# Kernel optimization log

Measured on AMD Instinct MI355X. Metric: run time of the kernel, lower is better.

## Reference

```python
import jax, jax.numpy as jnp
import numpy as np

B = 131072
H_GAS = 8
H_EXT = 16
# gas order and net counts, total 99 tiny MLPs
GAS_SIZES = [23, 29, 13, 9, 3, 9, 13]  # h2o, h2o_sq, o3, co2, n2o, ch4, u
N_NETS = 29

# index maps taken verbatim from the 29 tau_gases assignment lines
H2O_ROWS = np.arange(23)
H2O_IDX = np.array([0,1,2,3,4,5,6,3,4,9,10,11,12,13,14,15,16,17,18,19,20,21,22])
O3_ROWS = np.array([0,1,2,17,18,19,20,21,22,25,26,27,28])
CO2_ROWS = np.array([0,1,2,5,6,9,10,13,14])
N2O_ROWS = np.array([0,1,2])
CH4_ROWS = np.array([0,1,2,3,4,7,8,11,12])
U_ROWS = np.array([0,1,2,15,16,17,18,19,20,21,22,27,28])


def setup_inputs() -> dict:
    key = jax.random.key(0)
    ks = jax.random.split(key, 23)
    f = jnp.float32
    inp = {
        'temp': jax.random.normal(ks[0], (B, 1), f),
        'pressure': jax.random.normal(ks[1], (B, 1), f),
        'comp_h2o': jax.random.uniform(ks[2], (B, 1), f),
        'comp_h2o_sq': jax.random.uniform(ks[3], (B, 1), f),
        'comp_o3': jax.random.uniform(ks[4], (B, 1), f),
        'comp_co2': jax.random.uniform(ks[5], (B, 1), f),
        'comp_n2o': jax.random.uniform(ks[6], (B, 1), f),
        'comp_ch4': jax.random.uniform(ks[7], (B, 1), f),
        'comp_u': jax.random.uniform(ks[8], (B, 1), f),
        'lwp': jax.random.uniform(ks[9], (B, 1), f, minval=0.05, maxval=1.0),
        'iwp': jax.random.uniform(ks[10], (B, 1), f, minval=0.05, maxval=1.0),
        'mu': jax.random.uniform(ks[11], (B, 1), f, minval=0.1, maxval=1.0),
        'mu_bar': jax.random.uniform(ks[12], (B, 1), f, minval=0.1, maxval=1.0),
        'gas_W1': jax.random.normal(ks[13], (99, 2, H_GAS), f) * 0.5,
        'gas_b1': jax.random.normal(ks[14], (99, H_GAS), f) * 0.1,
        'gas_W2': jax.random.normal(ks[15], (99, H_GAS, 1), f) * 0.5,
        'gas_b2': jax.random.uniform(ks[16], (99, 1), f, minval=0.05, maxval=0.5),
        'lw_w': jax.random.uniform(ks[17], (N_NETS, 1), f, minval=0.05, maxval=1.0),
        'iw_w': jax.random.uniform(ks[18], (N_NETS, 1), f, minval=0.05, maxval=1.0),
        'ext_W1': jax.random.normal(ks[19], (N_NETS, 4, H_EXT), f) * 0.5,
        'ext_b1': jax.random.normal(ks[20], (N_NETS, H_EXT), f) * 0.1,
        'ext_W2': jax.random.normal(ks[21], (N_NETS, H_EXT, 3), f) * 0.5,
        'ext_b2': jax.random.normal(ks[22], (N_NETS, 3), f) * 0.1,
    }
    return inp


def reference(temp, pressure, comp_h2o, comp_h2o_sq, comp_o3, comp_co2, comp_n2o,
              comp_ch4, comp_u, lwp, iwp, mu, mu_bar,
              gas_W1, gas_b1, gas_W2, gas_b2, lw_w, iw_w,
              ext_W1, ext_b1, ext_W2, ext_b2):
    b = temp.shape[0]
    X = jnp.concatenate([temp, pressure], axis=-1)              # [B,2]
    # all 99 per-gas tiny MLPs in one batched pass
    h = jax.nn.elu(jnp.einsum('bi,nih->nbh', X, gas_W1) + gas_b1[:, None, :])
    ke = jax.nn.relu(jnp.einsum('nbh,nho->nbo', h, gas_W2) + gas_b2[:, None, :])[..., 0]  # [99,B]
    comps = [comp_h2o, comp_h2o_sq, comp_o3, comp_co2, comp_n2o, comp_ch4, comp_u]
    comp_all = jnp.concatenate(
        [jnp.broadcast_to(c[:, 0][None, :], (n, b)) for c, n in zip(comps, GAS_SIZES)], axis=0)
    tau_all = ke * comp_all                                      # [99,B]
    h2o    = tau_all[0:23]
    h2o_sq = tau_all[23:52]
    o3     = tau_all[52:65]
    co2    = tau_all[65:74]
    n2o    = tau_all[74:77]
    ch4    = tau_all[77:86]
    u      = tau_all[86:99]
    # scatter-combine into the 29 spectral channels
    tau_g = h2o_sq                                               # every row has h2o_sq[k]
    tau_g = tau_g.at[H2O_ROWS].add(h2o[H2O_IDX])
    tau_g = tau_g.at[O3_ROWS].add(o3)
    tau_g = tau_g.at[CO2_ROWS].add(co2)
    tau_g = tau_g.at[N2O_ROWS].add(n2o)
    tau_g = tau_g.at[CH4_ROWS].add(ch4)
    tau_g = tau_g.at[U_ROWS].add(u)
    tau_lw = lw_w * lwp[:, 0][None, :]                           # [29,B]
    tau_iw = iw_w * iwp[:, 0][None, :]
    tau_total = tau_g + tau_lw + tau_iw
    in1 = tau_lw / tau_total
    in2 = tau_iw / tau_total
    mu_v, mub_v = mu[:, 0], mu_bar[:, 0]
    in3_dir = tau_total / mu_v[None, :]
    in3_dif = tau_total / mub_v[None, :]

    def ext(i1, i2, i3, m):
        Xe = jnp.stack([i1, i2, i3, jnp.broadcast_to(m[None, :], i1.shape)], axis=-1)  # [29,B,4]
        he = jax.nn.elu(jnp.einsum('nbi,nih->nbh', Xe, ext_W1) + ext_b1[:, None, :])
        return jax.nn.relu(jnp.einsum('nbh,nho->nbo', he, ext_W2) + ext_b2[:, None, :])

    e_direct = jax.nn.softmax(ext(in1, in2, in3_dir, mu_v), axis=-1)   # [29,B,3]
    e_diffuse = jax.nn.softmax(ext(in1, in2, in3_dif, mub_v), axis=-1)
    t_direct = jnp.exp(-in3_dir)
    t_diffuse = jnp.exp(-in3_dif)
    return (t_direct, t_diffuse, e_direct, e_diffuse)
```

## Files before the change

kernel.cpp:

```cpp
#include <hip/hip_runtime.h>
#include <math.h>

#define TPB 256

static __device__ const int ROW_START[30] = {
    0, 7, 14, 21, 24, 27, 30, 33, 36, 39, 42, 45, 48, 51, 54, 57, 60,
    63, 67, 71, 75, 79, 83, 87, 88, 89, 91, 93, 96, 99};

static __device__ const unsigned char NET_ID[99] = {
    23, 0, 52, 65, 74, 77, 86,
    24, 1, 53, 66, 75, 78, 87,
    25, 2, 54, 67, 76, 79, 88,
    26, 3, 80,
    27, 4, 81,
    28, 5, 68,
    29, 6, 69,
    30, 3, 82,
    31, 4, 83,
    32, 9, 70,
    33, 10, 71,
    34, 11, 84,
    35, 12, 85,
    36, 13, 72,
    37, 14, 73,
    38, 15, 89,
    39, 16, 90,
    40, 17, 55, 91,
    41, 18, 56, 92,
    42, 19, 57, 93,
    43, 20, 58, 94,
    44, 21, 59, 95,
    45, 22, 60, 96,
    46,
    47,
    48, 61,
    49, 62,
    50, 63, 97,
    51, 64, 98};

static __device__ const unsigned char COMP_ID[99] = {
    1, 0, 2, 3, 4, 5, 6,
    1, 0, 2, 3, 4, 5, 6,
    1, 0, 2, 3, 4, 5, 6,
    1, 0, 5,
    1, 0, 5,
    1, 0, 3,
    1, 0, 3,
    1, 0, 5,
    1, 0, 5,
    1, 0, 3,
    1, 0, 3,
    1, 0, 5,
    1, 0, 5,
    1, 0, 3,
    1, 0, 3,
    1, 0, 6,
    1, 0, 6,
    1, 0, 2, 6,
    1, 0, 2, 6,
    1, 0, 2, 6,
    1, 0, 2, 6,
    1, 0, 2, 6,
    1, 0, 2, 6,
    1,
    1,
    1, 2,
    1, 2,
    1, 2, 6,
    1, 2, 6};

__device__ __forceinline__ float fast_rcp(float x) {
    return __builtin_amdgcn_rcpf(x);
}

__global__ __launch_bounds__(TPB) void atm_kernel(
    const float* __restrict__ temp,
    const float* __restrict__ pressure,
    const float* __restrict__ c_h2o,
    const float* __restrict__ c_h2o_sq,
    const float* __restrict__ c_o3,
    const float* __restrict__ c_co2,
    const float* __restrict__ c_n2o,
    const float* __restrict__ c_ch4,
    const float* __restrict__ c_u,
    const float* __restrict__ lwp,
    const float* __restrict__ iwp,
    const float* __restrict__ mu,
    const float* __restrict__ mu_bar,
    const float* __restrict__ gW1,
    const float* __restrict__ gb1,
    const float* __restrict__ gW2,
    const float* __restrict__ gb2,
    const float* __restrict__ lw_w,
    const float* __restrict__ iw_w,
    const float* __restrict__ eW1,
    const float* __restrict__ eb1,
    const float* __restrict__ eW2,
    const float* __restrict__ eb2,
    float* __restrict__ out,
    int Bn)
{
    const int r = blockIdx.x;
    const int b = blockIdx.y * TPB + threadIdx.x;
    if (b >= Bn) return;

    const float t = temp[b];
    const float p = pressure[b];
    float comp[7];
    comp[0] = c_h2o[b];
    comp[1] = c_h2o_sq[b];
    comp[2] = c_o3[b];
    comp[3] = c_co2[b];
    comp[4] = c_n2o[b];
    comp[5] = c_ch4[b];
    comp[6] = c_u[b];
    const float lwp_b = lwp[b], iwp_b = iwp[b];
    const float mu_b = mu[b], mub_b = mu_bar[b];

    float tau_g = 0.f;
    const int i0 = ROW_START[r], i1 = ROW_START[r + 1];
    for (int i = i0; i < i1; ++i) {
        const int n = NET_ID[i];
        const float* w1 = gW1 + n * 16;
        const float* b1 = gb1 + n * 8;
        const float* w2 = gW2 + n * 8;
        float acc = gb2[n];
        #pragma unroll
        for (int j = 0; j < 8; ++j) {
            float h = fmaf(t, w1[j], fmaf(p, w1[8 + j], b1[j]));
            h = h > 0.f ? h : (__expf(h) - 1.f);
            acc = fmaf(h, w2[j], acc);
        }
        acc = fmaxf(acc, 0.f);
        tau_g = fmaf(acc, comp[COMP_ID[i]], tau_g);
    }

    const float tlw = lw_w[r] * lwp_b;
    const float tiw = iw_w[r] * iwp_b;
    const float tau_tot = tau_g + tlw + tiw;
    const float inv_tt = fast_rcp(tau_tot);
    const float in1 = tlw * inv_tt;
    const float in2 = tiw * inv_tt;
    const float in3_dir = tau_tot * fast_rcp(mu_b);
    const float in3_dif = tau_tot * fast_rcp(mub_b);

    const size_t idx = (size_t)r * (size_t)Bn + (size_t)b;
    out[idx] = __expf(-in3_dir);
    out[(size_t)29 * Bn + idx] = __expf(-in3_dif);

    const float* w1 = eW1 + r * 64;
    const float* b1 = eb1 + r * 16;
    const float* w2 = eW2 + r * 48;
    const float* b2 = eb2 + r * 3;

    float res[6];
    #pragma unroll
    for (int pass = 0; pass < 2; ++pass) {
        const float i3 = (pass == 0) ? in3_dir : in3_dif;
        const float m  = (pass == 0) ? mu_b : mub_b;
        float o0 = b2[0], o1 = b2[1], o2 = b2[2];
        #pragma unroll
        for (int j = 0; j < 16; ++j) {
            float h = fmaf(in1, w1[j], b1[j]);
            h = fmaf(in2, w1[16 + j], h);
            h = fmaf(i3,  w1[32 + j], h);
            h = fmaf(m,   w1[48 + j], h);
            h = h > 0.f ? h : (__expf(h) - 1.f);
            o0 = fmaf(h, w2[3 * j + 0], o0);
            o1 = fmaf(h, w2[3 * j + 1], o1);
            o2 = fmaf(h, w2[3 * j + 2], o2);
        }
        o0 = fmaxf(o0, 0.f);
        o1 = fmaxf(o1, 0.f);
        o2 = fmaxf(o2, 0.f);
        const float mx = fmaxf(o0, fmaxf(o1, o2));
        const float e0 = __expf(o0 - mx);
        const float e1 = __expf(o1 - mx);
        const float e2 = __expf(o2 - mx);
        const float rs = fast_rcp(e0 + e1 + e2);
        res[pass * 3 + 0] = e0 * rs;
        res[pass * 3 + 1] = e1 * rs;
        res[pass * 3 + 2] = e2 * rs;
    }

    float* pd = out + (size_t)58 * Bn + idx * 3;
    pd[0] = res[0]; pd[1] = res[1]; pd[2] = res[2];
    float* pf = out + (size_t)145 * Bn + idx * 3;
    pf[0] = res[3]; pf[1] = res[4]; pf[2] = res[5];
}

extern "C" void kernel_launch(void* const* d_in, const int* in_sizes, int n_in,
                              void* d_out, int out_size, void* d_ws, size_t ws_size,
                              hipStream_t stream) {
    const int Bn = in_sizes[0];
    dim3 grid(29, (Bn + TPB - 1) / TPB);
    atm_kernel<<<grid, TPB, 0, stream>>>(
        (const float*)d_in[0],  (const float*)d_in[1],  (const float*)d_in[2],
        (const float*)d_in[3],  (const float*)d_in[4],  (const float*)d_in[5],
        (const float*)d_in[6],  (const float*)d_in[7],  (const float*)d_in[8],
        (const float*)d_in[9],  (const float*)d_in[10], (const float*)d_in[11],
        (const float*)d_in[12], (const float*)d_in[13], (const float*)d_in[14],
        (const float*)d_in[15], (const float*)d_in[16], (const float*)d_in[17],
        (const float*)d_in[18], (const float*)d_in[19], (const float*)d_in[20],
        (const float*)d_in[21], (const float*)d_in[22],
        (float*)d_out, Bn);
}
```

Measured before the change: 225.7 us.

## Process two batch elements per thread with vectorized weight loads and shared ext first layer

Each thread now handles two batch elements, so weight loads (now float4) are amortized across both and across the direct/diffuse passes. The per-row net list is a fixed 8-slot table indexed by component, which removes the COMP_ID indirection and allows full unrolling. In the ext MLP the in1/in2/bias part of the hidden pre-activation is computed once and reused by the direct and diffuse paths. The cost is higher register pressure and half as many blocks, which lowers occupancy.

```diff
diff --git a/kernel.cpp b/kernel.cpp
--- a/kernel.cpp
+++ b/kernel.cpp
@@ -2,75 +2,60 @@
 #include <math.h>
 
 #define TPB 256
-
-static __device__ const int ROW_START[30] = {
-    0, 7, 14, 21, 24, 27, 30, 33, 36, 39, 42, 45, 48, 51, 54, 57, 60,
-    63, 67, 71, 75, 79, 83, 87, 88, 89, 91, 93, 96, 99};
-
-static __device__ const unsigned char NET_ID[99] = {
-    23, 0, 52, 65, 74, 77, 86,
-    24, 1, 53, 66, 75, 78, 87,
-    25, 2, 54, 67, 76, 79, 88,
-    26, 3, 80,
-    27, 4, 81,
-    28, 5, 68,
-    29, 6, 69,
-    30, 3, 82,
-    31, 4, 83,
-    32, 9, 70,
-    33, 10, 71,
-    34, 11, 84,
-    35, 12, 85,
-    36, 13, 72,
-    37, 14, 73,
-    38, 15, 89,
-    39, 16, 90,
-    40, 17, 55, 91,
-    41, 18, 56, 92,
-    42, 19, 57, 93,
-    43, 20, 58, 94,
-    44, 21, 59, 95,
-    45, 22, 60, 96,
-    46,
-    47,
-    48, 61,
-    49, 62,
-    50, 63, 97,
-    51, 64, 98};
-
-static __device__ const unsigned char COMP_ID[99] = {
-    1, 0, 2, 3, 4, 5, 6,
-    1, 0, 2, 3, 4, 5, 6,
-    1, 0, 2, 3, 4, 5, 6,
-    1, 0, 5,
-    1, 0, 5,
-    1, 0, 3,
-    1, 0, 3,
-    1, 0, 5,
-    1, 0, 5,
-    1, 0, 3,
-    1, 0, 3,
-    1, 0, 5,
-    1, 0, 5,
-    1, 0, 3,
-    1, 0, 3,
-    1, 0, 6,
-    1, 0, 6,
-    1, 0, 2, 6,
-    1, 0, 2, 6,
-    1, 0, 2, 6,
-    1, 0, 2, 6,
-    1, 0, 2, 6,
-    1, 0, 2, 6,
-    1,
-    1,
-    1, 2,
-    1, 2,
-    1, 2, 6,
-    1, 2, 6};
+#define EPT 2
+
+static __device__ const unsigned char NETS[29][8] = {
+    {  0, 23,  52,  65,  74,  77,  86, 255},
+    {  1, 24,  53,  66,  75,  78,  87, 255},
+    {  2, 25,  54,  67,  76,  79,  88, 255},
+    {  3, 26, 255, 255, 255,  80, 255, 255},
+    {  4, 27, 255, 255, 255,  81, 255, 255},
+    {  5, 28, 255,  68, 255, 255, 255, 255},
+    {  6, 29, 255,  69, 255, 255, 255, 255},
+    {  3, 30, 255, 255, 255,  82, 255, 255},
+    {  4, 31, 255, 255, 255,  83, 255, 255},
+    {  9, 32, 255,  70, 255, 255, 255, 255},
+    { 10, 33, 255,  71, 255, 255, 255, 255},
+    { 11, 34, 255, 255, 255,  84, 255, 255},
+    { 12, 35, 255, 255, 255,  85, 255, 255},
+    { 13, 36, 255,  72, 255, 255, 255, 255},
+    { 14, 37, 255,  73, 255, 255, 255, 255},
+    { 15, 38, 255, 255, 255, 255,  89, 255},
+    { 16, 39, 255, 255, 255, 255,  90, 255},
+    { 17, 40,  55, 255, 255, 255,  91, 255},
+    { 18, 41,  56, 255, 255, 255,  92, 255},
+    { 19, 42,  57, 255, 255, 255,  93, 255},
+    { 20, 43,  58, 255, 255, 255,  94, 255},
+    { 21, 44,  59, 255, 255, 255,  95, 255},
+    { 22, 45,  60, 255, 255, 255,  96, 255},
+    {255, 46, 255, 255, 255, 255, 255, 255},
+    {255, 47, 255, 255, 255, 255, 255, 255},
+    {255, 48,  61, 255, 255, 255, 255, 255},
+    {255, 49,  62, 255, 255, 255, 255, 255},
+    {255, 50,  63, 255, 255, 255,  97, 255},
+    {255, 51,  64, 255, 255, 255,  98, 255}};
+
+__device__ __forceinline__ float elu1(float h) {
+    return h > 0.f ? h : (__expf(h) - 1.f);
+}
 
 __device__ __forceinline__ float fast_rcp(float x) {
     return __builtin_amdgcn_rcpf(x);
+}
+
+__device__ __forceinline__ void softmax3_store(float o0, float o1, float o2,
+                                               float* __restrict__ dst) {
+    o0 = fmaxf(o0, 0.f);
+    o1 = fmaxf(o1, 0.f);
+    o2 = fmaxf(o2, 0.f);
+    const float mx = fmaxf(o0, fmaxf(o1, o2));
+    const float e0 = __expf(o0 - mx);
+    const float e1 = __expf(o1 - mx);
+    const float e2 = __expf(o2 - mx);
+    const float rs = fast_rcp(e0 + e1 + e2);
+    dst[0] = e0 * rs;
+    dst[1] = e1 * rs;
+    dst[2] = e2 * rs;
 }
 
 __global__ __launch_bounds__(TPB) void atm_kernel(
@@ -101,99 +86,142 @@
     int Bn)
 {
     const int r = blockIdx.x;
-    const int b = blockIdx.y * TPB + threadIdx.x;
-    if (b >= Bn) return;
-
-    const float t = temp[b];
-    const float p = pressure[b];
-    float comp[7];
-    comp[0] = c_h2o[b];
-    comp[1] = c_h2o_sq[b];
-    comp[2] = c_o3[b];
-    comp[3] = c_co2[b];
-    comp[4] = c_n2o[b];
-    comp[5] = c_ch4[b];
-    comp[6] = c_u[b];
-    const float lwp_b = lwp[b], iwp_b = iwp[b];
-    const float mu_b = mu[b], mub_b = mu_bar[b];
-
-    float tau_g = 0.f;
-    const int i0 = ROW_START[r], i1 = ROW_START[r + 1];
-    for (int i = i0; i < i1; ++i) {
-        const int n = NET_ID[i];
-        const float* w1 = gW1 + n * 16;
-        const float* b1 = gb1 + n * 8;
-        const float* w2 = gW2 + n * 8;
-        float acc = gb2[n];
-        #pragma unroll
-        for (int j = 0; j < 8; ++j) {
-            float h = fmaf(t, w1[j], fmaf(p, w1[8 + j], b1[j]));
-            h = h > 0.f ? h : (__expf(h) - 1.f);
-            acc = fmaf(h, w2[j], acc);
+    const int base = blockIdx.y * (TPB * EPT) + threadIdx.x;
+    if (base >= Bn) return;
+    const int bA = base;
+    const int bB = base + TPB;
+    const bool vB = (bB < Bn);
+    const int bBl = vB ? bB : bA;
+
+    const float tA = temp[bA],       tB = temp[bBl];
+    const float pA = pressure[bA],   pB = pressure[bBl];
+    float cA[7], cB[7];
+    cA[0] = c_h2o[bA];     cB[0] = c_h2o[bBl];
+    cA[1] = c_h2o_sq[bA];  cB[1] = c_h2o_sq[bBl];
+    cA[2] = c_o3[bA];      cB[2] = c_o3[bBl];
+    cA[3] = c_co2[bA];     cB[3] = c_co2[bBl];
+    cA[4] = c_n2o[bA];     cB[4] = c_n2o[bBl];
+    cA[5] = c_ch4[bA];     cB[5] = c_ch4[bBl];
+    cA[6] = c_u[bA];       cB[6] = c_u[bBl];
+    const float lwpA = lwp[bA],    lwpB = lwp[bBl];
+    const float iwpA = iwp[bA],    iwpB = iwp[bBl];
+    const float muA  = mu[bA],     muB  = mu[bBl];
+    const float mbA  = mu_bar[bA], mbB  = mu_bar[bBl];
+
+    float tgA = 0.f, tgB = 0.f;
+    #pragma unroll
+    for (int s = 0; s < 7; ++s) {
+        const int n = NETS[r][s];
+        if (n != 255) {
+            const float4* W1 = (const float4*)(gW1 + (n << 4));
+            const float4 wt0 = W1[0], wt1 = W1[1];
+            const float4 wp0 = W1[2], wp1 = W1[3];
+            const float4* B1 = (const float4*)(gb1 + (n << 3));
+            const float4 bb0 = B1[0], bb1 = B1[1];
+            const float4* W2 = (const float4*)(gW2 + (n << 3));
+            const float4 wo0 = W2[0], wo1 = W2[1];
+            const float bias = gb2[n];
+            float aA = bias, aB = bias;
+#define GAS_H(WT, WP, BB, WO, K)                                        \
+            { float hA = fmaf(tA, (WT).K, fmaf(pA, (WP).K, (BB).K));    \
+              float hB = fmaf(tB, (WT).K, fmaf(pB, (WP).K, (BB).K));    \
+              hA = elu1(hA); hB = elu1(hB);                             \
+              aA = fmaf(hA, (WO).K, aA); aB = fmaf(hB, (WO).K, aB); }
+            GAS_H(wt0, wp0, bb0, wo0, x)
+            GAS_H(wt0, wp0, bb0, wo0, y)
+            GAS_H(wt0, wp0, bb0, wo0, z)
+            GAS_H(wt0, wp0, bb0, wo0, w)
+            GAS_H(wt1, wp1, bb1, wo1, x)
+            GAS_H(wt1, wp1, bb1, wo1, y)
+            GAS_H(wt1, wp1, bb1, wo1, z)
+            GAS_H(wt1, wp1, bb1, wo1, w)
+#undef GAS_H
+            aA = fmaxf(aA, 0.f);
+            aB = fmaxf(aB, 0.f);
+            tgA = fmaf(aA, cA[s], tgA);
+            tgB = fmaf(aB, cB[s], tgB);
         }
-        acc = fmaxf(acc, 0.f);
-        tau_g = fmaf(acc, comp[COMP_ID[i]], tau_g);
-    }
-
-    const float tlw = lw_w[r] * lwp_b;
-    const float tiw = iw_w[r] * iwp_b;
-    const float tau_tot = tau_g + tlw + tiw;
-    const float inv_tt = fast_rcp(tau_tot);
-    const float in1 = tlw * inv_tt;
-    const float in2 = tiw * inv_tt;
-    const float in3_dir = tau_tot * fast_rcp(mu_b);
-    const float in3_dif = tau_tot * fast_rcp(mub_b);
-
-    const size_t idx = (size_t)r * (size_t)Bn + (size_t)b;
-    out[idx] = __expf(-in3_dir);
-    out[(size_t)29 * Bn + idx] = __expf(-in3_dif);
-
-    const float* w1 = eW1 + r * 64;
-    const float* b1 = eb1 + r * 16;
-    const float* w2 = eW2 + r * 48;
-    const float* b2 = eb2 + r * 3;
-
-    float res[6];
+    }
+
+    const float lwr = lw_w[r], iwr = iw_w[r];
+    const float tlwA = lwr * lwpA, tlwB = lwr * lwpB;
+    const float tiwA = iwr * iwpA, tiwB = iwr * iwpB;
+    const float ttA = tgA + tlwA + tiwA;
+    const float ttB = tgB + tlwB + tiwB;
+    const float rttA = fast_rcp(ttA);
+    const float rttB = fast_rcp(ttB);
+    const float in1A = tlwA * rttA, in2A = tiwA * rttA;
+    const float in1B = tlwB * rttB, in2B = tiwB * rttB;
+    const float i3dA = ttA * fast_rcp(muA);
+    const float i3fA = ttA * fast_rcp(mbA);
+    const float i3dB = ttB * fast_rcp(muB);
+    const float i3fB = ttB * fast_rcp(mbB);
+
+    const size_t idxA = (size_t)r * (size_t)Bn + (size_t)bA;
+    out[idxA] = __expf(-i3dA);
+    out[(size_t)29 * Bn + idxA] = __expf(-i3fA);
+    if (vB) {
+        out[idxA + TPB] = __expf(-i3dB);
+        out[(size_t)29 * Bn + idxA + TPB] = __expf(-i3fB);
+    }
+
+    const float* w1  = eW1 + (r << 6);
+    const float* ebv = eb1 + (r << 4);
+    const float* w2  = eW2 + r * 48;
+    const float bo0 = eb2[r * 3 + 0];
+    const float bo1 = eb2[r * 3 + 1];
+    const float bo2 = eb2[r * 3 + 2];
+
+    float dA0 = bo0, dA1 = bo1, dA2 = bo2;
+    float fA0 = bo0, fA1 = bo1, fA2 = bo2;
+    float dB0 = bo0, dB1 = bo1, dB2 = bo2;
+    float fB0 = bo0, fB1 = bo1, fB2 = bo2;
+
     #pragma unroll
-    for (int pass = 0; pass < 2; ++pass) {
-        const float i3 = (pass == 0) ? in3_dir : in3_dif;
-        const float m  = (pass == 0) ? mu_b : mub_b;
-        float o0 = b2[0], o1 = b2[1], o2 = b2[2];
-        #pragma unroll
-        for (int j = 0; j < 16; ++j) {
-            float h = fmaf(in1, w1[j], b1[j]);
-            h = fmaf(in2, w1[16 + j], h);
-            h = fmaf(i3,  w1[32 + j], h);
-            h = fmaf(m,   w1[48 + j], h);
-            h = h > 0.f ? h : (__expf(h) - 1.f);
-            o0 = fmaf(h, w2[3 * j + 0], o0);
-            o1 = fmaf(h, w2[3 * j + 1], o1);
-            o2 = fmaf(h, w2[3 * j + 2], o2);
-        }
-        o0 = fmaxf(o0, 0.f);
-        o1 = fmaxf(o1, 0.f);
-        o2 = fmaxf(o2, 0.f);
-        const float mx = fmaxf(o0, fmaxf(o1, o2));
-        const float e0 = __expf(o0 - mx);
-        const float e1 = __expf(o1 - mx);
-        const float e2 = __expf(o2 - mx);
-        const float rs = fast_rcp(e0 + e1 + e2);
-        res[pass * 3 + 0] = e0 * rs;
-        res[pass * 3 + 1] = e1 * rs;
-        res[pass * 3 + 2] = e2 * rs;
-    }
-
-    float* pd = out + (size_t)58 * Bn + idx * 3;
-    pd[0] = res[0]; pd[1] = res[1]; pd[2] = res[2];
-    float* pf = out + (size_t)145 * Bn + idx * 3;
-    pf[0] = res[3]; pf[1] = res[4]; pf[2] = res[5];
+    for (int q = 0; q < 4; ++q) {
+        const float4 wA4 = *(const float4*)(w1 + 4 * q);
+        const float4 wB4 = *(const float4*)(w1 + 16 + 4 * q);
+        const float4 wC4 = *(const float4*)(w1 + 32 + 4 * q);
+        const float4 wD4 = *(const float4*)(w1 + 48 + 4 * q);
+        const float4 bj4 = *(const float4*)(ebv + 4 * q);
+        const float4 u0  = *(const float4*)(w2 + 12 * q);
+        const float4 u1  = *(const float4*)(w2 + 12 * q + 4);
+        const float4 u2  = *(const float4*)(w2 + 12 * q + 8);
+#define EXT_H(K, W20, W21, W22)                                               \
+        { const float bsA = fmaf(in1A, (wA4).K, fmaf(in2A, (wB4).K, (bj4).K)); \
+          const float bsB = fmaf(in1B, (wA4).K, fmaf(in2B, (wB4).K, (bj4).K)); \
+          const float hdA = elu1(fmaf(i3dA, (wC4).K, fmaf(muA, (wD4).K, bsA))); \
+          const float hfA = elu1(fmaf(i3fA, (wC4).K, fmaf(mbA, (wD4).K, bsA))); \
+          const float hdB = elu1(fmaf(i3dB, (wC4).K, fmaf(muB, (wD4).K, bsB))); \
+          const float hfB = elu1(fmaf(i3fB, (wC4).K, fmaf(mbB, (wD4).K, bsB))); \
+          dA0 = fmaf(hdA, (W20), dA0); dA1 = fmaf(hdA, (W21), dA1); dA2 = fmaf(hdA, (W22), dA2); \
+          fA0 = fmaf(hfA, (W20), fA0); fA1 = fmaf(hfA, (W21), fA1); fA2 = fmaf(hfA, (W22), fA2); \
+          dB0 = fmaf(hdB, (W20), dB0); dB1 = fmaf(hdB, (W21), dB1); dB2 = fmaf(hdB, (W22), dB2); \
+          fB0 = fmaf(hfB, (W20), fB0); fB1 = fmaf(hfB, (W21), fB1); fB2 = fmaf(hfB, (W22), fB2); }
+        EXT_H(x, u0.x, u0.y, u0.z)
+        EXT_H(y, u0.w, u1.x, u1.y)
+        EXT_H(z, u1.z, u1.w, u2.x)
+        EXT_H(w, u2.y, u2.z, u2.w)
+#undef EXT_H
+    }
+
+    float* pdA = out + (size_t)58 * Bn + idxA * 3;
+    float* pfA = out + (size_t)145 * Bn + idxA * 3;
+    softmax3_store(dA0, dA1, dA2, pdA);
+    softmax3_store(fA0, fA1, fA2, pfA);
+    if (vB) {
+        float* pdB = out + (size_t)58 * Bn + (idxA + TPB) * 3;
+        float* pfB = out + (size_t)145 * Bn + (idxA + TPB) * 3;
+        softmax3_store(dB0, dB1, dB2, pdB);
+        softmax3_store(fB0, fB1, fB2, pfB);
+    }
 }
 
 extern "C" void kernel_launch(void* const* d_in, const int* in_sizes, int n_in,
                               void* d_out, int out_size, void* d_ws, size_t ws_size,
                               hipStream_t stream) {
     const int Bn = in_sizes[0];
-    dim3 grid(29, (Bn + TPB - 1) / TPB);
+    dim3 grid(29, (Bn + TPB * EPT - 1) / (TPB * EPT));
     atm_kernel<<<grid, TPB, 0, stream>>>(
         (const float*)d_in[0],  (const float*)d_in[1],  (const float*)d_in[2],
         (const float*)d_in[3],  (const float*)d_in[4],  (const float*)d_in[5],
```

New measurement: 224.5 us. About the same (-0.5%).
